# Kernel optimization log

Hardware: AMD Instinct MI355X
Metric: run time of the kernel (lower is better)

Reference implementation:

```python
import jax, jax.numpy as jnp
import numpy as np
import math

S, E = 4096, 2048
H = 4 * E  # FFN hidden
EPS = 1e-5


def _ln_all(y):
    # F.layer_norm(y, y.shape): normalize over ALL elements, no affine
    mu = jnp.mean(y)
    var = jnp.mean(jnp.square(y - mu))
    return (y - mu) / jnp.sqrt(var + EPS)


def setup_inputs() -> dict:
    key = jax.random.key(0)
    ks = jax.random.split(key, 12)
    sc = 0.02
    return {
        "x": jax.random.normal(ks[0], (S, E), dtype=jnp.float32),
        "Wq": jax.random.normal(ks[1], (E, E), dtype=jnp.float32) * sc,
        "bq": jnp.zeros((E,), dtype=jnp.float32),
        "Wk": jax.random.normal(ks[2], (E, E), dtype=jnp.float32) * sc,
        "bk": jnp.zeros((E,), dtype=jnp.float32),
        "Wv": jax.random.normal(ks[3], (E, E), dtype=jnp.float32) * sc,
        "bv": jnp.zeros((E,), dtype=jnp.float32),
        "W1": jax.random.normal(ks[4], (E, H), dtype=jnp.float32) * sc,
        "b1": jnp.zeros((H,), dtype=jnp.float32),
        "W2": jax.random.normal(ks[5], (H, E), dtype=jnp.float32) * sc,
        "b2": jnp.zeros((E,), dtype=jnp.float32),
    }


def reference(x, Wq, bq, Wk, bk, Wv, bv, W1, b1, W2, b2):
    # projections
    Q = x @ Wq + bq  # [S, E]
    K = x @ Wk + bk
    V = x @ Wv + bv
    # NOTE: source scales by sqrt(K.size(-2)) == sqrt(seq_len), not head dim
    scale = 1.0 / math.sqrt(x.shape[-2])
    scores = jax.nn.softmax((Q @ K.T) * scale, axis=-1)  # [S, S]
    attn = scores @ V  # [S, E]
    h = _ln_all(x + attn)
    ffn = jax.nn.relu(h @ W1 + b1) @ W2 + b2
    return _ln_all(h + ffn)
```

## Files before the change

### kernel.cpp

```cpp
#include <hip/hip_runtime.h>
#include <cstdint>
#include <cstddef>


constexpr int S = 4096;
constexpr int E = 2048;
constexpr int H = 8192;

typedef __bf16 bf16;
typedef bf16  bf16x8 __attribute__((ext_vector_type(8)));
typedef bf16  bf16x4 __attribute__((ext_vector_type(4)));
typedef float f32x4  __attribute__((ext_vector_type(4)));

typedef __attribute__((address_space(1))) void as1_void;
typedef __attribute__((address_space(3))) void as3_void;

__device__ __forceinline__ void ldg2lds16(const void* g, void* l) {
  __builtin_amdgcn_global_load_lds((as1_void*)g, (as3_void*)l, 16, 0, 0);
}

template <int EPI>
__global__ __launch_bounds__(512, 2)
void gemm8(const bf16* __restrict__ A, int lda,
           const bf16* __restrict__ Bt, int ldb,
           bf16* __restrict__ Cb, float* __restrict__ Cf, int ldc,
           const float* __restrict__ bias, const float* __restrict__ add,
           const bf16* __restrict__ addb,
           float* __restrict__ red, int M, int N, int K, float scale)
{
  __shared__ bf16 sA[2][128 * 64];
  __shared__ bf16 sB[2][256 * 64];

  const int tid  = threadIdx.x;
  const int lane = tid & 63;
  const int wave = tid >> 6;

  const int nbx = gridDim.x;
  const int nwg = nbx * gridDim.y;
  const int bid = blockIdx.y * nbx + blockIdx.x;
  const int wg  = (bid & 7) * (nwg >> 3) + (bid >> 3);
  const int m0  = (wg / nbx) * 128;
  const int n0  = (wg % nbx) * 256;

  const int wm = (wave & 1) * 64;
  const int wn = (wave >> 1) * 64;

  const int tr  = tid >> 3;
  const int tc  = tid & 7;
  const int gsw = (tc ^ (tr & 7)) * 8;
  const bf16* gA = A  + (size_t)(m0 + tr) * lda + gsw;
  const bf16* gB = Bt + (size_t)(n0 + tr) * ldb + gsw;
  const size_t a64 = (size_t)64 * lda;
  const size_t b64 = (size_t)64 * ldb;

  const int fr = lane & 15;
  const int fq = lane >> 4;
  const int p0 = (fq ^ (fr & 7)) * 8;
  const int p1 = p0 ^ 32;

  const int NT = K >> 6;

  ldg2lds16(gA,             &sA[0][tid * 8]);
  ldg2lds16(gA + a64,       &sA[0][4096  + tid * 8]);
  ldg2lds16(gB,             &sB[0][tid * 8]);
  ldg2lds16(gB + b64,       &sB[0][4096  + tid * 8]);
  ldg2lds16(gB + 2 * b64,   &sB[0][8192  + tid * 8]);
  ldg2lds16(gB + 3 * b64,   &sB[0][12288 + tid * 8]);
  ldg2lds16(gA + 64,        &sA[1][tid * 8]);
  ldg2lds16(gA + 64 + a64,  &sA[1][4096  + tid * 8]);
  asm volatile("s_waitcnt vmcnt(2)" ::: "memory");
  __builtin_amdgcn_s_barrier();

  f32x4 acc[4][4] = {};

  for (int t = 0; t < NT; ++t) {
    const int bu = t & 1, nx = bu ^ 1;
    const bf16* rA = &sA[bu][(wm + fr) * 64];
    const bf16* rB = &sB[bu][(wn + fr) * 64];
    bf16x8 aF0[2], aF1[2], bF0[4], bF1[4];

    aF0[0] = *(const bf16x8*)(rA + p0);
    aF1[0] = *(const bf16x8*)(rA + p1);
    aF0[1] = *(const bf16x8*)(rA + 1024 + p0);
    aF1[1] = *(const bf16x8*)(rA + 1024 + p1);
    bF0[0] = *(const bf16x8*)(rB + p0);
    bF1[0] = *(const bf16x8*)(rB + p1);
    bF0[1] = *(const bf16x8*)(rB + 1024 + p0);
    bF1[1] = *(const bf16x8*)(rB + 1024 + p1);
    if (t + 1 < NT) {
      const bf16* g = gB + ((size_t)(t + 1) << 6);
      ldg2lds16(g,       &sB[nx][tid * 8]);
      ldg2lds16(g + b64, &sB[nx][4096 + tid * 8]);
    }
    __builtin_amdgcn_s_barrier();
    asm volatile("s_waitcnt lgkmcnt(0)" ::: "memory");
    __builtin_amdgcn_s_setprio(1);
#pragma unroll
    for (int i = 0; i < 2; ++i)
#pragma unroll
      for (int j = 0; j < 2; ++j) {
        acc[i][j] = __builtin_amdgcn_mfma_f32_16x16x32_bf16(aF0[i], bF0[j], acc[i][j], 0, 0, 0);
        acc[i][j] = __builtin_amdgcn_mfma_f32_16x16x32_bf16(aF1[i], bF1[j], acc[i][j], 0, 0, 0);
      }
    __builtin_amdgcn_s_setprio(0);
    __builtin_amdgcn_s_barrier();

    bF0[2] = *(const bf16x8*)(rB + 2048 + p0);
    bF1[2] = *(const bf16x8*)(rB + 2048 + p1);
    bF0[3] = *(const bf16x8*)(rB + 3072 + p0);
    bF1[3] = *(const bf16x8*)(rB + 3072 + p1);
    if (t + 1 < NT) {
      const bf16* g = gB + ((size_t)(t + 1) << 6) + 2 * b64;
      ldg2lds16(g,       &sB[nx][8192  + tid * 8]);
      ldg2lds16(g + b64, &sB[nx][12288 + tid * 8]);
    }
    __builtin_amdgcn_s_barrier();
    asm volatile("s_waitcnt lgkmcnt(0)" ::: "memory");
    __builtin_amdgcn_s_setprio(1);
#pragma unroll
    for (int i = 0; i < 2; ++i)
#pragma unroll
      for (int j = 0; j < 2; ++j) {
        acc[i][2 + j] = __builtin_amdgcn_mfma_f32_16x16x32_bf16(aF0[i], bF0[2 + j], acc[i][2 + j], 0, 0, 0);
        acc[i][2 + j] = __builtin_amdgcn_mfma_f32_16x16x32_bf16(aF1[i], bF1[2 + j], acc[i][2 + j], 0, 0, 0);
      }
    __builtin_amdgcn_s_setprio(0);
    __builtin_amdgcn_s_barrier();

    aF0[0] = *(const bf16x8*)(rA + 2048 + p0);
    aF1[0] = *(const bf16x8*)(rA + 2048 + p1);
    aF0[1] = *(const bf16x8*)(rA + 3072 + p0);
    aF1[1] = *(const bf16x8*)(rA + 3072 + p1);
    __builtin_amdgcn_s_barrier();
    asm volatile("s_waitcnt lgkmcnt(0)" ::: "memory");
    __builtin_amdgcn_s_setprio(1);
#pragma unroll
    for (int i = 0; i < 2; ++i)
#pragma unroll
      for (int j = 0; j < 2; ++j) {
        acc[2 + i][j] = __builtin_amdgcn_mfma_f32_16x16x32_bf16(aF0[i], bF0[j], acc[2 + i][j], 0, 0, 0);
        acc[2 + i][j] = __builtin_amdgcn_mfma_f32_16x16x32_bf16(aF1[i], bF1[j], acc[2 + i][j], 0, 0, 0);
      }
    __builtin_amdgcn_s_setprio(0);
    __builtin_amdgcn_s_barrier();

    if (t + 2 < NT) {
      const bf16* g = gA + ((size_t)(t + 2) << 6);
      ldg2lds16(g,       &sA[bu][tid * 8]);
      ldg2lds16(g + a64, &sA[bu][4096 + tid * 8]);
    }
    __builtin_amdgcn_s_barrier();
    __builtin_amdgcn_s_setprio(1);
#pragma unroll
    for (int i = 0; i < 2; ++i)
#pragma unroll
      for (int j = 0; j < 2; ++j) {
        acc[2 + i][2 + j] = __builtin_amdgcn_mfma_f32_16x16x32_bf16(aF0[i], bF0[2 + j], acc[2 + i][2 + j], 0, 0, 0);
        acc[2 + i][2 + j] = __builtin_amdgcn_mfma_f32_16x16x32_bf16(aF1[i], bF1[2 + j], acc[2 + i][2 + j], 0, 0, 0);
      }
    __builtin_amdgcn_s_setprio(0);
    if (t + 2 < NT) {
      asm volatile("s_waitcnt vmcnt(2)" ::: "memory");
    } else {
      asm volatile("s_waitcnt vmcnt(0)" ::: "memory");
    }
    __builtin_amdgcn_s_barrier();
  }

  const int er = m0 + wm + fq * 4;
  const int ec = n0 + wn + fr;
  float ls = 0.f, ls2 = 0.f;
#pragma unroll
  for (int i = 0; i < 4; ++i) {
#pragma unroll
    for (int r = 0; r < 4; ++r) {
      const int gr = er + i * 16 + r;
#pragma unroll
      for (int j = 0; j < 4; ++j) {
        const int gc = ec + j * 16;
        const size_t idx = (size_t)gr * ldc + gc;
        float v = acc[i][j][r];
        if (EPI == 0) {
          v += bias[gc];
          Cb[idx] = (bf16)v;
        } else if (EPI == 1) {
          v += bias[gr];
          Cb[idx] = (bf16)v;
        } else if (EPI == 2) {
          Cb[idx] = (bf16)(v * scale);
        } else if (EPI == 3) {
          v += add[idx];
          Cf[idx] = v; ls += v; ls2 += v * v;
        } else if (EPI == 4) {
          v += bias[gc];
          v = v > 0.f ? v : 0.f;
          Cb[idx] = (bf16)v;
        } else {
          v += bias[gc] + (float)addb[idx];
          Cf[idx] = v; ls += v; ls2 += v * v;
        }
      }
    }
  }

  if (EPI == 3 || EPI == 5) {
#pragma unroll
    for (int o = 32; o; o >>= 1) {
      ls  += __shfl_xor(ls,  o, 64);
      ls2 += __shfl_xor(ls2, o, 64);
    }
    float* sred = (float*)sA;
    if (lane == 0) { sred[wave * 2] = ls; sred[wave * 2 + 1] = ls2; }
    __syncthreads();
    if (tid == 0) {
      float a = 0.f, b = 0.f;
#pragma unroll
      for (int w = 0; w < 8; ++w) { a += sred[w * 2]; b += sred[w * 2 + 1]; }
      atomicAdd(red,     a);
      atomicAdd(red + 1, b);
    }
  }
}

__global__ __launch_bounds__(256)
void cvt_f32_bf16(const float* __restrict__ src, bf16* __restrict__ dst)
{
  const size_t i = ((size_t)blockIdx.x * 256 + threadIdx.x) * 4;
  const float4 t = *(const float4*)(src + i);
  bf16x4 b;
  b[0] = (bf16)t.x; b[1] = (bf16)t.y; b[2] = (bf16)t.z; b[3] = (bf16)t.w;
  *(bf16x4*)(dst + i) = b;
}

__global__ __launch_bounds__(256)
void transpose_cvt(const float* __restrict__ src, bf16* __restrict__ dst, int R, int C)
{
  __shared__ float tile[32][33];
  const int c0 = blockIdx.x * 32, r0 = blockIdx.y * 32;
  const int tx = threadIdx.x & 31, ty = threadIdx.x >> 5;
#pragma unroll
  for (int rr = ty; rr < 32; rr += 8)
    tile[rr][tx] = src[(size_t)(r0 + rr) * C + (c0 + tx)];
  __syncthreads();
#pragma unroll
  for (int rr = ty; rr < 32; rr += 8)
    dst[(size_t)(c0 + rr) * R + (r0 + tx)] = (bf16)tile[tx][rr];
}

__global__ __launch_bounds__(256)
void softmax_rows(bf16* __restrict__ P)
{
  const int row  = blockIdx.x;
  bf16* p = P + (size_t)row * 4096;
  const int tid  = threadIdx.x;
  const int lane = tid & 63, wave = tid >> 6;

  bf16x8 c0 = *(const bf16x8*)(p + tid * 16);
  bf16x8 c1 = *(const bf16x8*)(p + tid * 16 + 8);
  float v[16];
#pragma unroll
  for (int i = 0; i < 8; ++i) { v[i] = (float)c0[i]; v[8 + i] = (float)c1[i]; }

  float m = v[0];
#pragma unroll
  for (int i = 1; i < 16; ++i) m = fmaxf(m, v[i]);
#pragma unroll
  for (int o = 32; o; o >>= 1) m = fmaxf(m, __shfl_xor(m, o, 64));
  __shared__ float sred[8];
  if (lane == 0) sred[wave] = m;
  __syncthreads();
  m = fmaxf(fmaxf(sred[0], sred[1]), fmaxf(sred[2], sred[3]));

  float s = 0.f;
#pragma unroll
  for (int i = 0; i < 16; ++i) { v[i] = __expf(v[i] - m); s += v[i]; }
#pragma unroll
  for (int o = 32; o; o >>= 1) s += __shfl_xor(s, o, 64);
  if (lane == 0) sred[4 + wave] = s;
  __syncthreads();
  s = sred[4] + sred[5] + sred[6] + sred[7];

  const float inv = 1.f / s;
  bf16x8 o0, o1;
#pragma unroll
  for (int i = 0; i < 8; ++i) { o0[i] = (bf16)(v[i] * inv); o1[i] = (bf16)(v[8 + i] * inv); }
  *(bf16x8*)(p + tid * 16)     = o0;
  *(bf16x8*)(p + tid * 16 + 8) = o1;
}

__global__ void ln_finalize(float* red, float n)
{
  const float mu  = red[0] / n;
  const float var = red[1] / n - mu * mu;
  red[2] = mu;
  red[3] = rsqrtf(var + 1e-5f);
}

__global__ __launch_bounds__(256)
void ln_apply(const float* __restrict__ y, const float* __restrict__ red,
              float* __restrict__ of, bf16* __restrict__ ob)
{
  const float mu = red[2], rs = red[3];
  const size_t i = ((size_t)blockIdx.x * 256 + threadIdx.x) * 4;
  float4 t = *(const float4*)(y + i);
  t.x = (t.x - mu) * rs; t.y = (t.y - mu) * rs;
  t.z = (t.z - mu) * rs; t.w = (t.w - mu) * rs;
  if (of) *(float4*)(of + i) = t;
  if (ob) {
    bf16x4 b;
    b[0] = (bf16)t.x; b[1] = (bf16)t.y; b[2] = (bf16)t.z; b[3] = (bf16)t.w;
    *(bf16x4*)(ob + i) = b;
  }
}

extern "C" void kernel_launch(void* const* d_in, const int* in_sizes, int n_in,
                              void* d_out, int out_size, void* d_ws, size_t ws_size,
                              hipStream_t stream)
{
  const float* x  = (const float*)d_in[0];
  const float* Wq = (const float*)d_in[1];
  const float* bq = (const float*)d_in[2];
  const float* Wk = (const float*)d_in[3];
  const float* bk = (const float*)d_in[4];
  const float* Wv = (const float*)d_in[5];
  const float* bv = (const float*)d_in[6];
  const float* W1 = (const float*)d_in[7];
  const float* b1 = (const float*)d_in[8];
  const float* W2 = (const float*)d_in[9];
  const float* b2 = (const float*)d_in[10];
  float* out = (float*)d_out;

  const size_t MB = 1ull << 20;
  char* ws = (char*)d_ws;

  bf16*  xb  = (bf16*)(ws);
  bf16*  hb  = xb;
  bf16*  WqT = (bf16*)(ws + 16 * MB);
  bf16*  WkT = (bf16*)(ws + 24 * MB);
  bf16*  WvT = (bf16*)(ws + 32 * MB);
  bf16*  W1T = (bf16*)(ws + 40 * MB);
  bf16*  W2T = (bf16*)(ws + 72 * MB);
  bf16*  Qb  = (bf16*)(ws + 104 * MB);
  bf16*  Kb  = (bf16*)(ws + 120 * MB);
  bf16*  Pb  = (bf16*)(ws + 136 * MB);
  bf16*  act = (bf16*)(ws + 104 * MB);
  bf16*  VbT = (bf16*)(ws + 168 * MB);
  float* y   = (float*)(ws + 184 * MB);
  float* red = (float*)(ws + 216 * MB);

  hipMemsetAsync(red, 0, 32, stream);

  const dim3 blk(256);
  const dim3 blkg(512);
  const int nElemBlocks = (S * E) / 1024;

  cvt_f32_bf16<<<dim3(nElemBlocks), blk, 0, stream>>>(x, xb);
  transpose_cvt<<<dim3(E / 32, E / 32), blk, 0, stream>>>(Wq, WqT, E, E);
  transpose_cvt<<<dim3(E / 32, E / 32), blk, 0, stream>>>(Wk, WkT, E, E);
  transpose_cvt<<<dim3(E / 32, E / 32), blk, 0, stream>>>(Wv, WvT, E, E);
  transpose_cvt<<<dim3(H / 32, E / 32), blk, 0, stream>>>(W1, W1T, E, H);
  transpose_cvt<<<dim3(E / 32, H / 32), blk, 0, stream>>>(W2, W2T, H, E);

  gemm8<0><<<dim3(E / 256, S / 128), blkg, 0, stream>>>(
      xb, E, WqT, E, Qb, nullptr, E, bq, nullptr, nullptr, nullptr, S, E, E, 0.f);
  gemm8<0><<<dim3(E / 256, S / 128), blkg, 0, stream>>>(
      xb, E, WkT, E, Kb, nullptr, E, bk, nullptr, nullptr, nullptr, S, E, E, 0.f);
  gemm8<1><<<dim3(S / 256, E / 128), blkg, 0, stream>>>(
      WvT, E, xb, E, VbT, nullptr, S, bv, nullptr, nullptr, nullptr, E, S, E, 0.f);

  gemm8<2><<<dim3(S / 256, S / 128), blkg, 0, stream>>>(
      Qb, E, Kb, E, Pb, nullptr, S, nullptr, nullptr, nullptr, nullptr, S, S, E, 1.0f / 64.0f);
  softmax_rows<<<dim3(S), blk, 0, stream>>>(Pb);

  gemm8<3><<<dim3(E / 256, S / 128), blkg, 0, stream>>>(
      Pb, S, VbT, S, nullptr, y, E, nullptr, x, nullptr, red, S, E, S, 0.f);
  ln_finalize<<<1, 1, 0, stream>>>(red, (float)((size_t)S * E));
  ln_apply<<<dim3(nElemBlocks), blk, 0, stream>>>(y, red, nullptr, hb);

  gemm8<4><<<dim3(H / 256, S / 128), blkg, 0, stream>>>(
      hb, E, W1T, E, act, nullptr, H, b1, nullptr, nullptr, nullptr, S, H, E, 0.f);

  gemm8<5><<<dim3(E / 256, S / 128), blkg, 0, stream>>>(
      act, H, W2T, H, nullptr, y, E, b2, nullptr, hb, red + 4, S, E, H, 0.f);
  ln_finalize<<<1, 1, 0, stream>>>(red + 4, (float)((size_t)S * E));
  ln_apply<<<dim3(nElemBlocks), blk, 0, stream>>>(y, red + 4, out, nullptr);
}
```

Baseline: 1.005 ms.

## Use 256x256 GEMM tiles, fuse Q/K projection, split-K for narrow GEMMs

The GEMM tile grows from 128x256 to 256x256 per workgroup, with doubled A staging in LDS and twice as many accumulators per wave, to raise arithmetic intensity. Q and K projections are merged into one GEMM over a concatenated weight and bias. The N=2048 GEMMs (PV and FFN2) now use a 2-way split-K writing two fp32 partials, and a new combine_ln kernel sums them, adds the residual and bias, and accumulates the LayerNorm statistics. This keeps the machine busy despite fewer tiles, at the cost of extra fp32 partial traffic and higher register and LDS pressure, which may limit occupancy.

```diff
diff --git a/kernel.cpp b/kernel.cpp
--- a/kernel.cpp
+++ b/kernel.cpp
@@ -19,16 +19,16 @@
   __builtin_amdgcn_global_load_lds((as1_void*)g, (as3_void*)l, 16, 0, 0);
 }
 
-template <int EPI>
+template <int EPI, bool SPLITK>
 __global__ __launch_bounds__(512, 2)
-void gemm8(const bf16* __restrict__ A, int lda,
-           const bf16* __restrict__ Bt, int ldb,
-           bf16* __restrict__ Cb, float* __restrict__ Cf, int ldc,
-           const float* __restrict__ bias, const float* __restrict__ add,
-           const bf16* __restrict__ addb,
-           float* __restrict__ red, int M, int N, int K, float scale)
-{
-  __shared__ bf16 sA[2][128 * 64];
+void gemm256(const bf16* __restrict__ A, int lda,
+             const bf16* __restrict__ Bt, int ldb,
+             bf16* __restrict__ Cb, float* __restrict__ Cf,
+             float* __restrict__ Cf2, int ldc,
+             const float* __restrict__ bias,
+             int M, int N, int K, float scale)
+{
+  __shared__ bf16 sA[2][256 * 64];
   __shared__ bf16 sB[2][256 * 64];
 
   const int tid  = threadIdx.x;
@@ -38,12 +38,15 @@
   const int nbx = gridDim.x;
   const int nwg = nbx * gridDim.y;
   const int bid = blockIdx.y * nbx + blockIdx.x;
-  const int wg  = (bid & 7) * (nwg >> 3) + (bid >> 3);
-  const int m0  = (wg / nbx) * 128;
-  const int n0  = (wg % nbx) * 256;
-
-  const int wm = (wave & 1) * 64;
-  const int wn = (wave >> 1) * 64;
+  int wg = (bid & 7) * (nwg >> 3) + (bid >> 3);
+
+  int kh = 0;
+  if (SPLITK) { const int hw = nwg >> 1; if (wg >= hw) { kh = 1; wg -= hw; } }
+  const int ntx  = N >> 8;
+  const int m0   = (wg / ntx) * 256;
+  const int n0   = (wg % ntx) * 256;
+  const int Keff = SPLITK ? (K >> 1) : K;
+  if (SPLITK) { const size_t ko = (size_t)kh * Keff; A += ko; Bt += ko; }
 
   const int tr  = tid >> 3;
   const int tc  = tid & 7;
@@ -53,172 +56,198 @@
   const size_t a64 = (size_t)64 * lda;
   const size_t b64 = (size_t)64 * ldb;
 
+#define STAGE_A(t, g, b) ldg2lds16(gA + ((size_t)(t) << 6) + (size_t)(g) * a64, \
+                                   &sA[b][(g) * 4096 + tid * 8])
+#define STAGE_B(t, g, b) ldg2lds16(gB + ((size_t)(t) << 6) + (size_t)(g) * b64, \
+                                   &sB[b][(g) * 4096 + tid * 8])
+
   const int fr = lane & 15;
   const int fq = lane >> 4;
   const int p0 = (fq ^ (fr & 7)) * 8;
   const int p1 = p0 ^ 32;
-
-  const int NT = K >> 6;
-
-  ldg2lds16(gA,             &sA[0][tid * 8]);
-  ldg2lds16(gA + a64,       &sA[0][4096  + tid * 8]);
-  ldg2lds16(gB,             &sB[0][tid * 8]);
-  ldg2lds16(gB + b64,       &sB[0][4096  + tid * 8]);
-  ldg2lds16(gB + 2 * b64,   &sB[0][8192  + tid * 8]);
-  ldg2lds16(gB + 3 * b64,   &sB[0][12288 + tid * 8]);
-  ldg2lds16(gA + 64,        &sA[1][tid * 8]);
-  ldg2lds16(gA + 64 + a64,  &sA[1][4096  + tid * 8]);
-  asm volatile("s_waitcnt vmcnt(2)" ::: "memory");
+  const int wm = (wave & 1) * 128;
+  const int wn = (wave >> 1) * 64;
+
+  const int NT = Keff >> 6;
+
+  STAGE_A(0, 0, 0); STAGE_A(0, 1, 0); STAGE_A(0, 2, 0); STAGE_A(0, 3, 0);
+  STAGE_B(0, 0, 0); STAGE_B(0, 1, 0); STAGE_B(0, 2, 0); STAGE_B(0, 3, 0);
+  if (NT > 1) {
+    STAGE_A(1, 0, 1); STAGE_A(1, 2, 1);
+    STAGE_B(1, 0, 1); STAGE_B(1, 1, 1); STAGE_B(1, 2, 1); STAGE_B(1, 3, 1);
+    asm volatile("s_waitcnt vmcnt(6)" ::: "memory");
+  } else {
+    asm volatile("s_waitcnt vmcnt(0)" ::: "memory");
+  }
   __builtin_amdgcn_s_barrier();
 
-  f32x4 acc[4][4] = {};
+  f32x4 acc[8][4] = {};
 
   for (int t = 0; t < NT; ++t) {
     const int bu = t & 1, nx = bu ^ 1;
     const bf16* rA = &sA[bu][(wm + fr) * 64];
     const bf16* rB = &sB[bu][(wn + fr) * 64];
-    bf16x8 aF0[2], aF1[2], bF0[4], bF1[4];
-
-    aF0[0] = *(const bf16x8*)(rA + p0);
-    aF1[0] = *(const bf16x8*)(rA + p1);
-    aF0[1] = *(const bf16x8*)(rA + 1024 + p0);
-    aF1[1] = *(const bf16x8*)(rA + 1024 + p1);
-    bF0[0] = *(const bf16x8*)(rB + p0);
-    bF1[0] = *(const bf16x8*)(rB + p1);
-    bF0[1] = *(const bf16x8*)(rB + 1024 + p0);
-    bF1[1] = *(const bf16x8*)(rB + 1024 + p1);
-    if (t + 1 < NT) {
-      const bf16* g = gB + ((size_t)(t + 1) << 6);
-      ldg2lds16(g,       &sB[nx][tid * 8]);
-      ldg2lds16(g + b64, &sB[nx][4096 + tid * 8]);
-    }
+    bf16x8 a0[4], a1[4], bl0[2], bl1[2], bh0[2], bh1[2];
+
+#pragma unroll
+    for (int i = 0; i < 4; ++i) {
+      a0[i] = *(const bf16x8*)(rA + i * 1024 + p0);
+      a1[i] = *(const bf16x8*)(rA + i * 1024 + p1);
+    }
+#pragma unroll
+    for (int j = 0; j < 2; ++j) {
+      bl0[j] = *(const bf16x8*)(rB + j * 1024 + p0);
+      bl1[j] = *(const bf16x8*)(rB + j * 1024 + p1);
+    }
+    if (t + 1 < NT) { STAGE_A(t + 1, 1, nx); STAGE_A(t + 1, 3, nx); }
     __builtin_amdgcn_s_barrier();
     asm volatile("s_waitcnt lgkmcnt(0)" ::: "memory");
     __builtin_amdgcn_s_setprio(1);
 #pragma unroll
-    for (int i = 0; i < 2; ++i)
+    for (int i = 0; i < 4; ++i)
 #pragma unroll
       for (int j = 0; j < 2; ++j) {
-        acc[i][j] = __builtin_amdgcn_mfma_f32_16x16x32_bf16(aF0[i], bF0[j], acc[i][j], 0, 0, 0);
-        acc[i][j] = __builtin_amdgcn_mfma_f32_16x16x32_bf16(aF1[i], bF1[j], acc[i][j], 0, 0, 0);
+        acc[i][j] = __builtin_amdgcn_mfma_f32_16x16x32_bf16(a0[i], bl0[j], acc[i][j], 0, 0, 0);
+        acc[i][j] = __builtin_amdgcn_mfma_f32_16x16x32_bf16(a1[i], bl1[j], acc[i][j], 0, 0, 0);
       }
     __builtin_amdgcn_s_setprio(0);
     __builtin_amdgcn_s_barrier();
 
-    bF0[2] = *(const bf16x8*)(rB + 2048 + p0);
-    bF1[2] = *(const bf16x8*)(rB + 2048 + p1);
-    bF0[3] = *(const bf16x8*)(rB + 3072 + p0);
-    bF1[3] = *(const bf16x8*)(rB + 3072 + p1);
-    if (t + 1 < NT) {
-      const bf16* g = gB + ((size_t)(t + 1) << 6) + 2 * b64;
-      ldg2lds16(g,       &sB[nx][8192  + tid * 8]);
-      ldg2lds16(g + b64, &sB[nx][12288 + tid * 8]);
-    }
+#pragma unroll
+    for (int j = 0; j < 2; ++j) {
+      bh0[j] = *(const bf16x8*)(rB + (2 + j) * 1024 + p0);
+      bh1[j] = *(const bf16x8*)(rB + (2 + j) * 1024 + p1);
+    }
+    if (t + 2 < NT) { STAGE_A(t + 2, 0, bu); STAGE_A(t + 2, 2, bu); }
     __builtin_amdgcn_s_barrier();
     asm volatile("s_waitcnt lgkmcnt(0)" ::: "memory");
     __builtin_amdgcn_s_setprio(1);
 #pragma unroll
-    for (int i = 0; i < 2; ++i)
+    for (int i = 0; i < 4; ++i)
 #pragma unroll
       for (int j = 0; j < 2; ++j) {
-        acc[i][2 + j] = __builtin_amdgcn_mfma_f32_16x16x32_bf16(aF0[i], bF0[2 + j], acc[i][2 + j], 0, 0, 0);
-        acc[i][2 + j] = __builtin_amdgcn_mfma_f32_16x16x32_bf16(aF1[i], bF1[2 + j], acc[i][2 + j], 0, 0, 0);
+        acc[i][2 + j] = __builtin_amdgcn_mfma_f32_16x16x32_bf16(a0[i], bh0[j], acc[i][2 + j], 0, 0, 0);
+        acc[i][2 + j] = __builtin_amdgcn_mfma_f32_16x16x32_bf16(a1[i], bh1[j], acc[i][2 + j], 0, 0, 0);
       }
     __builtin_amdgcn_s_setprio(0);
     __builtin_amdgcn_s_barrier();
 
-    aF0[0] = *(const bf16x8*)(rA + 2048 + p0);
-    aF1[0] = *(const bf16x8*)(rA + 2048 + p1);
-    aF0[1] = *(const bf16x8*)(rA + 3072 + p0);
-    aF1[1] = *(const bf16x8*)(rA + 3072 + p1);
+#pragma unroll
+    for (int i = 0; i < 4; ++i) {
+      a0[i] = *(const bf16x8*)(rA + 4096 + i * 1024 + p0);
+      a1[i] = *(const bf16x8*)(rA + 4096 + i * 1024 + p1);
+    }
+    if (t + 2 < NT) { STAGE_B(t + 2, 0, bu); STAGE_B(t + 2, 1, bu); }
     __builtin_amdgcn_s_barrier();
     asm volatile("s_waitcnt lgkmcnt(0)" ::: "memory");
     __builtin_amdgcn_s_setprio(1);
 #pragma unroll
-    for (int i = 0; i < 2; ++i)
+    for (int i = 0; i < 4; ++i)
 #pragma unroll
       for (int j = 0; j < 2; ++j) {
-        acc[2 + i][j] = __builtin_amdgcn_mfma_f32_16x16x32_bf16(aF0[i], bF0[j], acc[2 + i][j], 0, 0, 0);
-        acc[2 + i][j] = __builtin_amdgcn_mfma_f32_16x16x32_bf16(aF1[i], bF1[j], acc[2 + i][j], 0, 0, 0);
+        acc[4 + i][2 + j] = __builtin_amdgcn_mfma_f32_16x16x32_bf16(a0[i], bh0[j], acc[4 + i][2 + j], 0, 0, 0);
+        acc[4 + i][2 + j] = __builtin_amdgcn_mfma_f32_16x16x32_bf16(a1[i], bh1[j], acc[4 + i][2 + j], 0, 0, 0);
       }
     __builtin_amdgcn_s_setprio(0);
     __builtin_amdgcn_s_barrier();
 
-    if (t + 2 < NT) {
-      const bf16* g = gA + ((size_t)(t + 2) << 6);
-      ldg2lds16(g,       &sA[bu][tid * 8]);
-      ldg2lds16(g + a64, &sA[bu][4096 + tid * 8]);
-    }
+    if (t + 2 < NT) { STAGE_B(t + 2, 2, bu); STAGE_B(t + 2, 3, bu); }
     __builtin_amdgcn_s_barrier();
     __builtin_amdgcn_s_setprio(1);
 #pragma unroll
-    for (int i = 0; i < 2; ++i)
+    for (int i = 0; i < 4; ++i)
 #pragma unroll
       for (int j = 0; j < 2; ++j) {
-        acc[2 + i][2 + j] = __builtin_amdgcn_mfma_f32_16x16x32_bf16(aF0[i], bF0[2 + j], acc[2 + i][2 + j], 0, 0, 0);
-        acc[2 + i][2 + j] = __builtin_amdgcn_mfma_f32_16x16x32_bf16(aF1[i], bF1[2 + j], acc[2 + i][2 + j], 0, 0, 0);
+        acc[4 + i][j] = __builtin_amdgcn_mfma_f32_16x16x32_bf16(a0[i], bl0[j], acc[4 + i][j], 0, 0, 0);
+        acc[4 + i][j] = __builtin_amdgcn_mfma_f32_16x16x32_bf16(a1[i], bl1[j], acc[4 + i][j], 0, 0, 0);
       }
     __builtin_amdgcn_s_setprio(0);
     if (t + 2 < NT) {
-      asm volatile("s_waitcnt vmcnt(2)" ::: "memory");
-    } else {
+      asm volatile("s_waitcnt vmcnt(6)" ::: "memory");
+    } else if (t + 1 < NT) {
       asm volatile("s_waitcnt vmcnt(0)" ::: "memory");
     }
     __builtin_amdgcn_s_barrier();
   }
+#undef STAGE_A
+#undef STAGE_B
 
   const int er = m0 + wm + fq * 4;
   const int ec = n0 + wn + fr;
-  float ls = 0.f, ls2 = 0.f;
-#pragma unroll
-  for (int i = 0; i < 4; ++i) {
-#pragma unroll
-    for (int r = 0; r < 4; ++r) {
-      const int gr = er + i * 16 + r;
-#pragma unroll
-      for (int j = 0; j < 4; ++j) {
-        const int gc = ec + j * 16;
-        const size_t idx = (size_t)gr * ldc + gc;
-        float v = acc[i][j][r];
-        if (EPI == 0) {
-          v += bias[gc];
-          Cb[idx] = (bf16)v;
-        } else if (EPI == 1) {
-          v += bias[gr];
-          Cb[idx] = (bf16)v;
-        } else if (EPI == 2) {
-          Cb[idx] = (bf16)(v * scale);
-        } else if (EPI == 3) {
-          v += add[idx];
-          Cf[idx] = v; ls += v; ls2 += v * v;
-        } else if (EPI == 4) {
-          v += bias[gc];
-          v = v > 0.f ? v : 0.f;
-          Cb[idx] = (bf16)v;
-        } else {
-          v += bias[gc] + (float)addb[idx];
-          Cf[idx] = v; ls += v; ls2 += v * v;
+  float* const dst6 = (EPI == 6) ? (kh ? Cf2 : Cf) : nullptr;
+#pragma unroll
+  for (int qm = 0; qm < 2; ++qm) {
+#pragma unroll
+    for (int i = 0; i < 4; ++i) {
+#pragma unroll
+      for (int r = 0; r < 4; ++r) {
+        const int gr = er + qm * 64 + i * 16 + r;
+#pragma unroll
+        for (int j = 0; j < 4; ++j) {
+          const int gc = ec + j * 16;
+          const size_t idx = (size_t)gr * ldc + gc;
+          float v = acc[qm * 4 + i][j][r];
+          if (EPI == 0) {
+            Cb[idx] = (bf16)(v + bias[gc]);
+          } else if (EPI == 1) {
+            Cb[idx] = (bf16)(v + bias[gr]);
+          } else if (EPI == 2) {
+            Cb[idx] = (bf16)(v * scale);
+          } else if (EPI == 4) {
+            v += bias[gc];
+            Cb[idx] = (bf16)(v > 0.f ? v : 0.f);
+          } else {
+            dst6[idx] = v;
+          }
         }
       }
     }
   }
-
-  if (EPI == 3 || EPI == 5) {
-#pragma unroll
-    for (int o = 32; o; o >>= 1) {
-      ls  += __shfl_xor(ls,  o, 64);
-      ls2 += __shfl_xor(ls2, o, 64);
-    }
-    float* sred = (float*)sA;
-    if (lane == 0) { sred[wave * 2] = ls; sred[wave * 2 + 1] = ls2; }
-    __syncthreads();
-    if (tid == 0) {
-      float a = 0.f, b = 0.f;
-#pragma unroll
-      for (int w = 0; w < 8; ++w) { a += sred[w * 2]; b += sred[w * 2 + 1]; }
-      atomicAdd(red,     a);
-      atomicAdd(red + 1, b);
-    }
+}
+
+__global__ __launch_bounds__(256)
+void combine_ln(const float* __restrict__ y0, const float* __restrict__ y1,
+                const float* __restrict__ bias, const float* __restrict__ addf,
+                const bf16* __restrict__ addb,
+                float* __restrict__ out, float* __restrict__ red,
+                int colMask, int total4)
+{
+  float ls = 0.f, ls2 = 0.f;
+  for (int idx = blockIdx.x * 256 + threadIdx.x; idx < total4;
+       idx += gridDim.x * 256) {
+    const size_t i = (size_t)idx * 4;
+    const float4 u0 = *(const float4*)(y0 + i);
+    const float4 u1 = *(const float4*)(y1 + i);
+    float vx = u0.x + u1.x, vy = u0.y + u1.y, vz = u0.z + u1.z, vw = u0.w + u1.w;
+    if (bias) {
+      const float4 b = *(const float4*)(bias + (int)(i & colMask));
+      vx += b.x; vy += b.y; vz += b.z; vw += b.w;
+    }
+    if (addf) {
+      const float4 a = *(const float4*)(addf + i);
+      vx += a.x; vy += a.y; vz += a.z; vw += a.w;
+    }
+    if (addb) {
+      const bf16x4 a = *(const bf16x4*)(addb + i);
+      vx += (float)a[0]; vy += (float)a[1]; vz += (float)a[2]; vw += (float)a[3];
+    }
+    float4 o; o.x = vx; o.y = vy; o.z = vz; o.w = vw;
+    *(float4*)(out + i) = o;
+    ls  += vx + vy + vz + vw;
+    ls2 += vx * vx + vy * vy + vz * vz + vw * vw;
+  }
+#pragma unroll
+  for (int o = 32; o; o >>= 1) {
+    ls  += __shfl_xor(ls,  o, 64);
+    ls2 += __shfl_xor(ls2, o, 64);
+  }
+  __shared__ float sr[8];
+  const int lane = threadIdx.x & 63, wave = threadIdx.x >> 6;
+  if (lane == 0) { sr[wave * 2] = ls; sr[wave * 2 + 1] = ls2; }
+  __syncthreads();
+  if (threadIdx.x == 0) {
+    atomicAdd(red,     sr[0] + sr[2] + sr[4] + sr[6]);
+    atomicAdd(red + 1, sr[1] + sr[3] + sr[5] + sr[7]);
   }
 }
 
@@ -245,6 +274,14 @@
 #pragma unroll
   for (int rr = ty; rr < 32; rr += 8)
     dst[(size_t)(c0 + rr) * R + (r0 + tx)] = (bf16)tile[tx][rr];
+}
+
+__global__ __launch_bounds__(256)
+void concat_bias(const float* __restrict__ a, const float* __restrict__ b,
+                 float* __restrict__ o)
+{
+  const int i = blockIdx.x * 256 + threadIdx.x;
+  o[i] = (i < 2048) ? a[i] : b[i - 2048];
 }
 
 __global__ __launch_bounds__(256)
@@ -333,55 +370,61 @@
   const size_t MB = 1ull << 20;
   char* ws = (char*)d_ws;
 
-  bf16*  xb  = (bf16*)(ws);
-  bf16*  hb  = xb;
-  bf16*  WqT = (bf16*)(ws + 16 * MB);
-  bf16*  WkT = (bf16*)(ws + 24 * MB);
-  bf16*  WvT = (bf16*)(ws + 32 * MB);
-  bf16*  W1T = (bf16*)(ws + 40 * MB);
-  bf16*  W2T = (bf16*)(ws + 72 * MB);
-  bf16*  Qb  = (bf16*)(ws + 104 * MB);
-  bf16*  Kb  = (bf16*)(ws + 120 * MB);
-  bf16*  Pb  = (bf16*)(ws + 136 * MB);
-  bf16*  act = (bf16*)(ws + 104 * MB);
-  bf16*  VbT = (bf16*)(ws + 168 * MB);
-  float* y   = (float*)(ws + 184 * MB);
-  float* red = (float*)(ws + 216 * MB);
+  bf16*  xb   = (bf16*)(ws);
+  bf16*  hb   = xb;
+  bf16*  WqkT = (bf16*)(ws + 16 * MB);
+  bf16*  WvT  = (bf16*)(ws + 32 * MB);
+  bf16*  W1T  = (bf16*)(ws + 40 * MB);
+  bf16*  W2T  = (bf16*)(ws + 72 * MB);
+  bf16*  QKb  = (bf16*)(ws + 104 * MB);
+  float* y1pv = (float*)(ws + 104 * MB);
+  bf16*  Pb   = (bf16*)(ws + 136 * MB);
+  bf16*  act  = (bf16*)(ws + 104 * MB);
+  bf16*  VbT  = (bf16*)(ws + 168 * MB);
+  float* y    = (float*)(ws + 184 * MB);
+  float* y1f2 = (float*)(ws + 16 * MB);
+  float* red  = (float*)(ws + 216 * MB);
+  float* bqk  = (float*)(ws + 216 * MB + 4096);
 
   hipMemsetAsync(red, 0, 32, stream);
 
   const dim3 blk(256);
   const dim3 blkg(512);
   const int nElemBlocks = (S * E) / 1024;
+  const int total4 = (S * E) / 4;
 
   cvt_f32_bf16<<<dim3(nElemBlocks), blk, 0, stream>>>(x, xb);
-  transpose_cvt<<<dim3(E / 32, E / 32), blk, 0, stream>>>(Wq, WqT, E, E);
-  transpose_cvt<<<dim3(E / 32, E / 32), blk, 0, stream>>>(Wk, WkT, E, E);
+  transpose_cvt<<<dim3(E / 32, E / 32), blk, 0, stream>>>(Wq, WqkT, E, E);
+  transpose_cvt<<<dim3(E / 32, E / 32), blk, 0, stream>>>(Wk, WqkT + (size_t)E * E, E, E);
   transpose_cvt<<<dim3(E / 32, E / 32), blk, 0, stream>>>(Wv, WvT, E, E);
   transpose_cvt<<<dim3(H / 32, E / 32), blk, 0, stream>>>(W1, W1T, E, H);
   transpose_cvt<<<dim3(E / 32, H / 32), blk, 0, stream>>>(W2, W2T, H, E);
-
-  gemm8<0><<<dim3(E / 256, S / 128), blkg, 0, stream>>>(
-      xb, E, WqT, E, Qb, nullptr, E, bq, nullptr, nullptr, nullptr, S, E, E, 0.f);
-  gemm8<0><<<dim3(E / 256, S / 128), blkg, 0, stream>>>(
-      xb, E, WkT, E, Kb, nullptr, E, bk, nullptr, nullptr, nullptr, S, E, E, 0.f);
-  gemm8<1><<<dim3(S / 256, E / 128), blkg, 0, stream>>>(
-      WvT, E, xb, E, VbT, nullptr, S, bv, nullptr, nullptr, nullptr, E, S, E, 0.f);
-
-  gemm8<2><<<dim3(S / 256, S / 128), blkg, 0, stream>>>(
-      Qb, E, Kb, E, Pb, nullptr, S, nullptr, nullptr, nullptr, nullptr, S, S, E, 1.0f / 64.0f);
+  concat_bias<<<dim3(16), blk, 0, stream>>>(bq, bk, bqk);
+
+  gemm256<0, false><<<dim3(4096 / 256, S / 256), blkg, 0, stream>>>(
+      xb, E, WqkT, E, QKb, nullptr, nullptr, 4096, bqk, S, 4096, E, 0.f);
+  gemm256<1, false><<<dim3(S / 256, E / 256), blkg, 0, stream>>>(
+      WvT, E, xb, E, VbT, nullptr, nullptr, S, bv, E, S, E, 0.f);
+
+  gemm256<2, false><<<dim3(S / 256, S / 256), blkg, 0, stream>>>(
+      QKb, 4096, QKb + 2048, 4096, Pb, nullptr, nullptr, S, nullptr,
+      S, S, E, 1.0f / 64.0f);
   softmax_rows<<<dim3(S), blk, 0, stream>>>(Pb);
 
-  gemm8<3><<<dim3(E / 256, S / 128), blkg, 0, stream>>>(
-      Pb, S, VbT, S, nullptr, y, E, nullptr, x, nullptr, red, S, E, S, 0.f);
+  gemm256<6, true><<<dim3(E / 256, (S / 256) * 2), blkg, 0, stream>>>(
+      Pb, S, VbT, S, nullptr, y, y1pv, E, nullptr, S, E, S, 0.f);
+  combine_ln<<<dim3(2048), blk, 0, stream>>>(
+      y, y1pv, nullptr, x, nullptr, y, red, E - 1, total4);
   ln_finalize<<<1, 1, 0, stream>>>(red, (float)((size_t)S * E));
   ln_apply<<<dim3(nElemBlocks), blk, 0, stream>>>(y, red, nullptr, hb);
 
-  gemm8<4><<<dim3(H / 256, S / 128), blkg, 0, stream>>>(
-      hb, E, W1T, E, act, nullptr, H, b1, nullptr, nullptr, nullptr, S, H, E, 0.f);
-
-  gemm8<5><<<dim3(E / 256, S / 128), blkg, 0, stream>>>(
-      act, H, W2T, H, nullptr, y, E, b2, nullptr, hb, red + 4, S, E, H, 0.f);
+  gemm256<4, false><<<dim3(H / 256, S / 256), blkg, 0, stream>>>(
+      hb, E, W1T, E, act, nullptr, nullptr, H, b1, S, H, E, 0.f);
+
+  gemm256<6, true><<<dim3(E / 256, (S / 256) * 2), blkg, 0, stream>>>(
+      act, H, W2T, H, nullptr, y, y1f2, E, nullptr, S, E, H, 0.f);
+  combine_ln<<<dim3(2048), blk, 0, stream>>>(
+      y, y1f2, b2, nullptr, hb, y, red + 4, E - 1, total4);
   ln_finalize<<<1, 1, 0, stream>>>(red + 4, (float)((size_t)S * E));
   ln_apply<<<dim3(nElemBlocks), blk, 0, stream>>>(y, red + 4, out, nullptr);
 }
```

Result: faster. 957.4 us (-4.8%).
